# Performance work log

Measured on AMD Instinct MI355X. Metric: run time of the kernel, lower is better.

The kernel has to match this reference:

```python
import jax, jax.numpy as jnp
import numpy as np
from functools import reduce

N_QUBITS = 5
DIM = 2 ** N_QUBITS  # 32


def _cnot_np(c, t):
    # CNOT on N_QUBITS qubits, wire 0 = most significant bit (deepquantum convention)
    M = np.zeros((DIM, DIM), np.complex64)
    for i in range(DIM):
        if (i >> (N_QUBITS - 1 - c)) & 1:
            j = i ^ (1 << (N_QUBITS - 1 - t))
        else:
            j = i
        M[j, i] = 1.0
    return M

_CNOT = {(c, t): jnp.asarray(_cnot_np(c, t))
         for c in range(N_QUBITS) for t in range(N_QUBITS) if c != t}
_EYE2 = jnp.eye(2, dtype=jnp.complex64)


def _ry(theta):
    c = jnp.cos(theta / 2).astype(jnp.complex64)
    s = jnp.sin(theta / 2).astype(jnp.complex64)
    return jnp.stack([jnp.stack([c, -s]), jnp.stack([s, c])])


def _rx(theta):
    c = jnp.cos(theta / 2).astype(jnp.complex64)
    s = jnp.sin(theta / 2).astype(jnp.complex64)
    js = jnp.complex64(1j) * s
    return jnp.stack([jnp.stack([c, -js]), jnp.stack([-js, c])])


def _layer(gate_fn, thetas, wires):
    # kron of single-qubit gates on `wires`, identity elsewhere
    mats, idx = [], 0
    for w in range(N_QUBITS):
        if w in wires:
            mats.append(gate_fn(thetas[idx])); idx += 1
        else:
            mats.append(_EYE2)
    return reduce(jnp.kron, mats)


def _build_circuit(params, wires):
    # params: (n_blocks, 2, len(wires)); block = rylayer, rxlayer, then CNOTs
    # with control = block index and targets = all other wires in increasing order
    U = jnp.eye(DIM, dtype=jnp.complex64)
    n_blocks = params.shape[0]
    for b in range(n_blocks):
        U = _layer(_ry, params[b, 0], wires) @ U
        U = _layer(_rx, params[b, 1], wires) @ U
        for t in wires:
            if t != b:
                U = _CNOT[(b, t)] @ U
    return U


def setup_inputs() -> dict:
    key = jax.random.key(0)
    k1, k2, k3 = jax.random.split(key, 3)
    B = 65536
    oracles = jax.random.normal(k1, (B, DIM, DIM), dtype=jnp.float32)
    params1 = jax.random.normal(k2, (5, 2, 5), dtype=jnp.float32)  # cir1: 5 blocks, ry+rx, 5 wires
    params2 = jax.random.normal(k3, (4, 2, 4), dtype=jnp.float32)  # cir2: 4 blocks, ry+rx, wires [0,1,2,3]
    return {"oracles": oracles, "params1": params1, "params2": params2}


def reference(oracles, params1, params2):
    U1 = _build_circuit(params1, [0, 1, 2, 3, 4])
    U2 = _build_circuit(params2, [0, 1, 2, 3])
    psi1 = U1[:, 0]  # cir1 applied to |00000>
    mid = jnp.einsum('bij,j->bi', oracles.astype(jnp.complex64), psi1)  # oracle application (batched)
    fin = jnp.einsum('ij,bj->bi', U2, mid)                              # cir2
    x = jnp.abs(fin[:, 0]) ** 2 + jnp.abs(fin[:, 1]) ** 2
    return jnp.stack([x, 1.0 - x], axis=-1)  # (B, 2)
```

## Files before the change

### kernel.cpp

```cpp
#include <hip/hip_runtime.h>
#include <math.h>


__device__ float g_coef[4096];

__device__ __forceinline__ void apply_ry(float c, float s, int mask, int lane,
                                         float& re, float& im) {
    float pre = __shfl_xor(re, mask, 64);
    float pim = __shfl_xor(im, mask, 64);
    float sg = (lane & mask) ? s : -s;
    re = c * re + sg * pre;
    im = c * im + sg * pim;
}

__device__ __forceinline__ void apply_rx(float c, float s, int mask,
                                         float& re, float& im) {
    float pre = __shfl_xor(re, mask, 64);
    float pim = __shfl_xor(im, mask, 64);
    float nre = c * re + s * pim;
    float nim = c * im - s * pre;
    re = nre; im = nim;
}

__device__ __forceinline__ void apply_cnot(int cmask, int tmask, int lane,
                                           float& re, float& im) {
    float pre = __shfl_xor(re, tmask, 64);
    float pim = __shfl_xor(im, tmask, 64);
    if (lane & cmask) { re = pre; im = pim; }
}

__global__ void setup_kernel(const float* __restrict__ p1,
                             const float* __restrict__ p2) {
    const int lane = threadIdx.x;
    const int l5 = lane & 31;
    __shared__ float sh[6][32];

    float re = (l5 == 0) ? 1.f : 0.f, im = 0.f;
    for (int b = 0; b < 5; ++b) {
        for (int w = 0; w < 5; ++w) {
            float s, c; __sincosf(p1[b * 10 + w] * 0.5f, &s, &c);
            apply_ry(c, s, 1 << (4 - w), lane, re, im);
        }
        for (int w = 0; w < 5; ++w) {
            float s, c; __sincosf(p1[b * 10 + 5 + w] * 0.5f, &s, &c);
            apply_rx(c, s, 1 << (4 - w), re, im);
        }
        for (int t = 0; t < 5; ++t)
            if (t != b) apply_cnot(1 << (4 - b), 1 << (4 - t), lane, re, im);
    }
    if (lane < 32) { sh[0][lane] = re; sh[1][lane] = im; }

    for (int r = 0; r < 2; ++r) {
        re = (l5 == r) ? 1.f : 0.f; im = 0.f;
        for (int b = 3; b >= 0; --b) {
            for (int t = 3; t >= 0; --t)
                if (t != b) apply_cnot(1 << (4 - b), 1 << (4 - t), lane, re, im);
            for (int w = 0; w < 4; ++w) {
                float s, c; __sincosf(p2[b * 8 + 4 + w] * 0.5f, &s, &c);
                apply_rx(c, s, 1 << (4 - w), re, im);
            }
            for (int w = 0; w < 4; ++w) {
                float s, c; __sincosf(p2[b * 8 + w] * 0.5f, &s, &c);
                apply_ry(c, -s, 1 << (4 - w), lane, re, im);
            }
        }
        if (lane < 32) { sh[2 + 2 * r][lane] = re; sh[3 + 2 * r][lane] = im; }
    }
    __syncthreads();

    for (int c = 0; c < 4; ++c) {
        for (int k = 0; k < 4; ++k) {
            int e = 256 * c + 4 * lane + k;
            int i = e >> 5, j = e & 31;
            float pr = sh[0][j], pi = sh[1][j];
            float ar = sh[2][i], ai = sh[3][i];
            float br = sh[4][i], bi = sh[5][i];
            float4 v;
            v.x = ar * pr - ai * pi;
            v.y = ar * pi + ai * pr;
            v.z = br * pr - bi * pi;
            v.w = br * pi + bi * pr;
            ((float4*)g_coef)[c * 256 + lane * 4 + k] = v;
        }
    }
}

__global__ __launch_bounds__(256, 4) void oracle_kernel(const float* __restrict__ O,
                                                        float* __restrict__ out,
                                                        int nbatch) {
    const int lane = threadIdx.x & 63;
    const int wid = blockIdx.x * (blockDim.x >> 6) + (threadIdx.x >> 6);
    const int nw = gridDim.x * (blockDim.x >> 6);

    float4 cf[4][4];
    const float4* cp = (const float4*)g_coef;
#pragma unroll
    for (int c = 0; c < 4; ++c)
#pragma unroll
        for (int k = 0; k < 4; ++k) cf[c][k] = cp[c * 256 + lane * 4 + k];

    int b = wid;
    if (b >= nbatch) return;

    float4 cur[4];
    {
        const float4* row = (const float4*)(O + (size_t)b * 1024);
#pragma unroll
        for (int c = 0; c < 4; ++c) cur[c] = row[c * 64 + lane];
    }

    while (true) {
        const int nb = b + nw;
        const bool more = nb < nbatch;
        float4 nxt[4];
        if (more) {
            const float4* row = (const float4*)(O + (size_t)nb * 1024);
#pragma unroll
            for (int c = 0; c < 4; ++c) nxt[c] = row[c * 64 + lane];
        }

        float a0 = 0.f, a1 = 0.f, a2 = 0.f, a3 = 0.f;
#pragma unroll
        for (int c = 0; c < 4; ++c) {
            float4 o = cur[c];
            a0 += o.x * cf[c][0].x + o.y * cf[c][1].x + o.z * cf[c][2].x + o.w * cf[c][3].x;
            a1 += o.x * cf[c][0].y + o.y * cf[c][1].y + o.z * cf[c][2].y + o.w * cf[c][3].y;
            a2 += o.x * cf[c][0].z + o.y * cf[c][1].z + o.z * cf[c][2].z + o.w * cf[c][3].z;
            a3 += o.x * cf[c][0].w + o.y * cf[c][1].w + o.z * cf[c][2].w + o.w * cf[c][3].w;
        }

        float v01 = (lane & 1) ? a1 : a0;
        float o01 = (lane & 1) ? a0 : a1;
        v01 += __shfl_xor(o01, 1, 64);
        float v23 = (lane & 1) ? a3 : a2;
        float o23 = (lane & 1) ? a2 : a3;
        v23 += __shfl_xor(o23, 1, 64);
        float v = (lane & 2) ? v23 : v01;
        float o = (lane & 2) ? v01 : v23;
        v += __shfl_xor(o, 2, 64);
#pragma unroll
        for (int m = 4; m < 64; m <<= 1) v += __shfl_xor(v, m, 64);
        float t = v * v;
        t += __shfl_xor(t, 1, 64);
        t += __shfl_xor(t, 2, 64);
        if (lane == 0) ((float2*)out)[b] = make_float2(t, 1.0f - t);

        if (!more) break;
        b = nb;
#pragma unroll
        for (int c = 0; c < 4; ++c) cur[c] = nxt[c];
    }
}

extern "C" void kernel_launch(void* const* d_in, const int* in_sizes, int n_in,
                              void* d_out, int out_size, void* d_ws, size_t ws_size,
                              hipStream_t stream) {
    const float* oracles = (const float*)d_in[0];
    const float* p1 = (const float*)d_in[1];
    const float* p2 = (const float*)d_in[2];
    float* out = (float*)d_out;
    int nbatch = in_sizes[0] / 1024;

    setup_kernel<<<1, 64, 0, stream>>>(p1, p2);
    oracle_kernel<<<2048, 256, 0, stream>>>(oracles, out, nbatch);
}
```

Baseline: 54.11 us.

## Fuse circuit setup into oracle kernel and overlap it with prefetch

```diff
diff --git a/kernel.cpp b/kernel.cpp
--- a/kernel.cpp
+++ b/kernel.cpp
@@ -1,8 +1,6 @@
 #include <hip/hip_runtime.h>
 #include <math.h>
 
-
-__device__ float g_coef[4096];
 
 __device__ __forceinline__ void apply_ry(float c, float s, int mask, int lane,
                                          float& re, float& im) {
@@ -29,96 +27,88 @@
     if (lane & cmask) { re = pre; im = pim; }
 }
 
-__global__ void setup_kernel(const float* __restrict__ p1,
-                             const float* __restrict__ p2) {
-    const int lane = threadIdx.x;
-    const int l5 = lane & 31;
-    __shared__ float sh[6][32];
-
-    float re = (l5 == 0) ? 1.f : 0.f, im = 0.f;
-    for (int b = 0; b < 5; ++b) {
-        for (int w = 0; w < 5; ++w) {
-            float s, c; __sincosf(p1[b * 10 + w] * 0.5f, &s, &c);
-            apply_ry(c, s, 1 << (4 - w), lane, re, im);
-        }
-        for (int w = 0; w < 5; ++w) {
-            float s, c; __sincosf(p1[b * 10 + 5 + w] * 0.5f, &s, &c);
+__device__ __forceinline__ void u2row(const float* __restrict__ p2, int r,
+                                      int lane, float& re, float& im) {
+    re = ((lane & 31) == r) ? 1.f : 0.f;
+    im = 0.f;
+    for (int b = 3; b >= 0; --b) {
+        for (int t = 3; t >= 0; --t)
+            if (t != b) apply_cnot(1 << (4 - b), 1 << (4 - t), lane, re, im);
+        for (int w = 0; w < 4; ++w) {
+            float s, c; __sincosf(p2[b * 8 + 4 + w] * 0.5f, &s, &c);
             apply_rx(c, s, 1 << (4 - w), re, im);
         }
-        for (int t = 0; t < 5; ++t)
-            if (t != b) apply_cnot(1 << (4 - b), 1 << (4 - t), lane, re, im);
-    }
-    if (lane < 32) { sh[0][lane] = re; sh[1][lane] = im; }
-
-    for (int r = 0; r < 2; ++r) {
-        re = (l5 == r) ? 1.f : 0.f; im = 0.f;
-        for (int b = 3; b >= 0; --b) {
-            for (int t = 3; t >= 0; --t)
-                if (t != b) apply_cnot(1 << (4 - b), 1 << (4 - t), lane, re, im);
-            for (int w = 0; w < 4; ++w) {
-                float s, c; __sincosf(p2[b * 8 + 4 + w] * 0.5f, &s, &c);
-                apply_rx(c, s, 1 << (4 - w), re, im);
-            }
-            for (int w = 0; w < 4; ++w) {
-                float s, c; __sincosf(p2[b * 8 + w] * 0.5f, &s, &c);
-                apply_ry(c, -s, 1 << (4 - w), lane, re, im);
-            }
-        }
-        if (lane < 32) { sh[2 + 2 * r][lane] = re; sh[3 + 2 * r][lane] = im; }
-    }
-    __syncthreads();
-
-    for (int c = 0; c < 4; ++c) {
-        for (int k = 0; k < 4; ++k) {
-            int e = 256 * c + 4 * lane + k;
-            int i = e >> 5, j = e & 31;
-            float pr = sh[0][j], pi = sh[1][j];
-            float ar = sh[2][i], ai = sh[3][i];
-            float br = sh[4][i], bi = sh[5][i];
-            float4 v;
-            v.x = ar * pr - ai * pi;
-            v.y = ar * pi + ai * pr;
-            v.z = br * pr - bi * pi;
-            v.w = br * pi + bi * pr;
-            ((float4*)g_coef)[c * 256 + lane * 4 + k] = v;
+        for (int w = 0; w < 4; ++w) {
+            float s, c; __sincosf(p2[b * 8 + w] * 0.5f, &s, &c);
+            apply_ry(c, -s, 1 << (4 - w), lane, re, im);
         }
     }
 }
 
-__global__ __launch_bounds__(256, 4) void oracle_kernel(const float* __restrict__ O,
-                                                        float* __restrict__ out,
-                                                        int nbatch) {
+__global__ __launch_bounds__(256, 4) void fused_kernel(const float* __restrict__ O,
+                                                       const float* __restrict__ p1,
+                                                       const float* __restrict__ p2,
+                                                       float* __restrict__ out,
+                                                       int nbatch) {
     const int lane = threadIdx.x & 63;
     const int wid = blockIdx.x * (blockDim.x >> 6) + (threadIdx.x >> 6);
     const int nw = gridDim.x * (blockDim.x >> 6);
 
-    float4 cf[4][4];
-    const float4* cp = (const float4*)g_coef;
-#pragma unroll
-    for (int c = 0; c < 4; ++c)
-#pragma unroll
-        for (int k = 0; k < 4; ++k) cf[c][k] = cp[c * 256 + lane * 4 + k];
-
     int b = wid;
-    if (b >= nbatch) return;
-
-    float4 cur[4];
-    {
+    float4 cur[4], nxt[4];
+    const bool has0 = b < nbatch;
+    const bool has1 = b + nw < nbatch;
+    if (has0) {
         const float4* row = (const float4*)(O + (size_t)b * 1024);
 #pragma unroll
         for (int c = 0; c < 4; ++c) cur[c] = row[c * 64 + lane];
     }
+    if (has1) {
+        const float4* row = (const float4*)(O + (size_t)(b + nw) * 1024);
+#pragma unroll
+        for (int c = 0; c < 4; ++c) nxt[c] = row[c * 64 + lane];
+    }
+
+    float p_re = ((lane & 31) == 0) ? 1.f : 0.f, p_im = 0.f;
+    for (int bb = 0; bb < 5; ++bb) {
+        for (int w = 0; w < 5; ++w) {
+            float s, c; __sincosf(p1[bb * 10 + w] * 0.5f, &s, &c);
+            apply_ry(c, s, 1 << (4 - w), lane, p_re, p_im);
+        }
+        for (int w = 0; w < 5; ++w) {
+            float s, c; __sincosf(p1[bb * 10 + 5 + w] * 0.5f, &s, &c);
+            apply_rx(c, s, 1 << (4 - w), p_re, p_im);
+        }
+        for (int t = 0; t < 5; ++t)
+            if (t != bb) apply_cnot(1 << (4 - bb), 1 << (4 - t), lane, p_re, p_im);
+    }
+    float r0re, r0im, r1re, r1im;
+    u2row(p2, 0, lane, r0re, r0im);
+    u2row(p2, 1, lane, r1re, r1im);
+
+    float4 cf[4][4];
+#pragma unroll
+    for (int k = 0; k < 4; ++k) {
+        const int e4 = 4 * lane + k;
+        const int j = e4 & 31;
+        const int tq = e4 >> 5;
+        float pr = __shfl(p_re, j, 64);
+        float pi = __shfl(p_im, j, 64);
+#pragma unroll
+        for (int c = 0; c < 4; ++c) {
+            const int i = 8 * c + tq;
+            float ar = __shfl(r0re, i, 64);
+            float ai = __shfl(r0im, i, 64);
+            float br = __shfl(r1re, i, 64);
+            float bi = __shfl(r1im, i, 64);
+            cf[c][k] = make_float4(ar * pr - ai * pi, ar * pi + ai * pr,
+                                   br * pr - bi * pi, br * pi + bi * pr);
+        }
+    }
+
+    if (!has0) return;
 
     while (true) {
-        const int nb = b + nw;
-        const bool more = nb < nbatch;
-        float4 nxt[4];
-        if (more) {
-            const float4* row = (const float4*)(O + (size_t)nb * 1024);
-#pragma unroll
-            for (int c = 0; c < 4; ++c) nxt[c] = row[c * 64 + lane];
-        }
-
         float a0 = 0.f, a1 = 0.f, a2 = 0.f, a3 = 0.f;
 #pragma unroll
         for (int c = 0; c < 4; ++c) {
@@ -136,19 +126,24 @@
         float o23 = (lane & 1) ? a2 : a3;
         v23 += __shfl_xor(o23, 1, 64);
         float v = (lane & 2) ? v23 : v01;
-        float o = (lane & 2) ? v01 : v23;
-        v += __shfl_xor(o, 2, 64);
+        float ov = (lane & 2) ? v01 : v23;
+        v += __shfl_xor(ov, 2, 64);
 #pragma unroll
         for (int m = 4; m < 64; m <<= 1) v += __shfl_xor(v, m, 64);
-        float t = v * v;
-        t += __shfl_xor(t, 1, 64);
-        t += __shfl_xor(t, 2, 64);
-        if (lane == 0) ((float2*)out)[b] = make_float2(t, 1.0f - t);
+        float x = v * v;
+        x += __shfl_xor(x, 1, 64);
+        x += __shfl_xor(x, 2, 64);
+        if (lane == 0) ((float2*)out)[b] = make_float2(x, 1.0f - x);
 
-        if (!more) break;
-        b = nb;
+        b += nw;
+        if (b >= nbatch) break;
 #pragma unroll
         for (int c = 0; c < 4; ++c) cur[c] = nxt[c];
+        if (b + nw < nbatch) {
+            const float4* row = (const float4*)(O + (size_t)(b + nw) * 1024);
+#pragma unroll
+            for (int c = 0; c < 4; ++c) nxt[c] = row[c * 64 + lane];
+        }
     }
 }
 
@@ -161,6 +156,5 @@
     float* out = (float*)d_out;
     int nbatch = in_sizes[0] / 1024;
 
-    setup_kernel<<<1, 64, 0, stream>>>(p1, p2);
-    oracle_kernel<<<2048, 256, 0, stream>>>(oracles, out, nbatch);
+    fused_kernel<<<1024, 256, 0, stream>>>(oracles, p1, p2, out, nbatch);
 }
```

Result: faster. 51.16 us (-5.5%).
